# Kernel optimization log

Hardware: AMD Instinct MI355X
Metric: run time of the kernel (lower is better)

The kernel has to match this reference:

```python
import jax, jax.numpy as jnp
import numpy as np

B, T, N = 1024, 256, 64  # batch, seq_len, n_labels


def setup_inputs() -> dict:
    key = jax.random.key(0)
    k1, k2, k3, k4, k5 = jax.random.split(key, 5)
    emit = jax.random.normal(k1, (B, T, N), dtype=jnp.float32)
    lens = jax.random.randint(k2, (B,), T // 2, T + 1)
    mask = jnp.arange(T)[None, :] < lens[:, None]  # [B, T] bool, monotone
    trans = 0.1 * jax.random.normal(k3, (N, N), dtype=jnp.float32)
    strans = 0.1 * jax.random.normal(k4, (N,), dtype=jnp.float32)
    etrans = 0.1 * jax.random.normal(k5, (N,), dtype=jnp.float32)
    return {"emit": emit, "trans": trans, "strans": strans,
            "etrans": etrans, "mask": mask}


def reference(emit, trans, strans, etrans, mask):
    """CRF partition function (Tagger.get_logZ), summed over the batch."""
    lse = jax.scipy.special.logsumexp
    # row-normalize transitions in log space (as in the torch module)
    strans_n = strans - lse(strans)
    etrans_n = etrans - lse(etrans)
    trans_n = trans - lse(trans, axis=-1, keepdims=True)  # [N, N]

    e = jnp.transpose(emit, (1, 0, 2))  # [T, B, N]
    m = mask.T                          # [T, B]

    alpha0 = strans_n + e[0]            # [B, N]

    def step(alpha, xs):
        emit_t, mask_t = xs             # [B, N], [B]
        # scores[b, k] = logsumexp_j(alpha[b, j] + trans[j, k] + emit_t[b, k])
        scores = lse(alpha[:, :, None] + trans_n[None, :, :]
                     + emit_t[:, None, :], axis=1)
        alpha = jnp.where(mask_t[:, None], scores, alpha)
        return alpha, None

    alpha, _ = jax.lax.scan(step, alpha0, (e[1:], m[1:]))
    logZ = jnp.sum(lse(alpha + etrans_n, axis=1))
    return logZ
```

## Files before the change

### kernel.cpp

```cpp
#include <hip/hip_runtime.h>


#define CRF_B 1024
#define CRF_T 256
#define CRF_N 64

typedef __bf16 bf16x2 __attribute__((ext_vector_type(2)));

__device__ __forceinline__ float rl0(float x) {
    return __int_as_float(__builtin_amdgcn_readfirstlane(__float_as_int(x)));
}
__device__ __forceinline__ float rlanef(float x, int j) {
    return __int_as_float(__builtin_amdgcn_readlane(__float_as_int(x), j));
}

__device__ __forceinline__ float wave_lse(float v) {
    float m = v;
    #pragma unroll
    for (int off = 1; off < 64; off <<= 1) m = fmaxf(m, __shfl_xor(m, off));
    float s = __expf(v - m);
    #pragma unroll
    for (int off = 1; off < 64; off <<= 1) s += __shfl_xor(s, off);
    return m + __logf(s);
}

__device__ __forceinline__ unsigned bf16_rne(float f) {
    unsigned u = __float_as_uint(f);
    return (u + 0x7FFFu + ((u >> 16) & 1u)) >> 16;
}

__device__ __forceinline__ unsigned pack_pairs(float u) {
    unsigned pa = __float_as_uint(u) + 0x8000u;
    unsigned pb = (unsigned)__builtin_amdgcn_update_dpp(
        0, (int)pa, 0xB1 , 0xF, 0xF, false);
    return __builtin_amdgcn_perm(pb, pa, 0x07060302);
}

__device__ __forceinline__ float dot2bf(unsigned a, unsigned b, float c) {
#if __has_builtin(__builtin_amdgcn_fdot2_f32_bf16)
    return __builtin_amdgcn_fdot2_f32_bf16(__builtin_bit_cast(bf16x2, a),
                                           __builtin_bit_cast(bf16x2, b),
                                           c, false);
#else
    float d = c;
    asm("v_dot2_f32_bf16 %0, %1, %2, %0" : "+v"(d) : "v"(a), "v"(b));
    return d;
#endif
}

__launch_bounds__(64, 1)
__global__ void crf_fwd_kernel(const float* __restrict__ emit,
                               const float* __restrict__ trans,
                               const float* __restrict__ strans,
                               const float* __restrict__ etrans,
                               const unsigned char* __restrict__ mask_u8,
                               float* __restrict__ out)
{
    const int lane = threadIdx.x;
    const int b    = blockIdx.x;

    float rowlse_v;
    {
        const float* rowp = trans + lane * CRF_N;
        float m = -1e30f;
        #pragma unroll 8
        for (int k = 0; k < CRF_N; ++k) m = fmaxf(m, rowp[k]);
        float s = 0.f;
        #pragma unroll 8
        for (int k = 0; k < CRF_N; ++k) s += __expf(rowp[k] - m);
        rowlse_v = m + __logf(s);
    }

    float cmx = -1e30f;
    #pragma unroll
    for (int j = 0; j < CRF_N; ++j)
        cmx = fmaxf(cmx, trans[j * CRF_N + lane] - rlanef(rowlse_v, j));

    unsigned Epk[32];
    #pragma unroll
    for (int m = 0; m < 32; ++m) {
        float e0 = __expf(trans[(2 * m)     * CRF_N + lane] - rlanef(rowlse_v, 2 * m)     - cmx);
        float e1 = __expf(trans[(2 * m + 1) * CRF_N + lane] - rlanef(rowlse_v, 2 * m + 1) - cmx);
        Epk[m] = bf16_rne(e0) | (bf16_rne(e1) << 16);
    }

    const float sn = wave_lse(strans[lane]);

    int len;
    {
        int c8 = 0;
        #pragma unroll
        for (int q = 0; q < 4; ++q)
            c8 += (mask_u8[(size_t)b * CRF_T + q * 64 + lane] != 0) ? 1 : 0;
        for (int off = 1; off < 64; off <<= 1) c8 += __shfl_xor(c8, off);
        if (c8 >= 128) {
            len = c8;
        } else {
            const int* mi = (const int*)mask_u8;
            int ci = 0;
            #pragma unroll
            for (int q = 0; q < 4; ++q)
                ci += (mi[(size_t)b * CRF_T + q * 64 + lane] != 0) ? 1 : 0;
            for (int off = 1; off < 64; off <<= 1) ci += __shfl_xor(ci, off);
            len = ci;
        }
    }

    const float* eb = emit + (size_t)b * CRF_T * CRF_N;

    float alpha0 = (strans[lane] - sn) + eb[lane];
    float c0 = rl0(alpha0);
    float u  = __expf(alpha0 - c0);
    unsigned upi = pack_pairs(u);
    float R  = 1.0f;
    float Pm = 1.0f;
    int   Eacc = 0;

#define CRF_STEP(EE, EE0)                                                   \
    {                                                                       \
        float ree = R * (EE);               \
        float sc0 = R * (EE0);                                              \
        float a0 = 0.f, a1 = 0.f, a2 = 0.f, a3 = 0.f;                       \
        _Pragma("unroll")                                                   \
        for (int m2 = 0; m2 < 32; m2 += 4) {                                \
            unsigned w0 = (unsigned)__builtin_amdgcn_readlane((int)upi, 2 * m2 + 0); \
            unsigned w1 = (unsigned)__builtin_amdgcn_readlane((int)upi, 2 * m2 + 2); \
            unsigned w2 = (unsigned)__builtin_amdgcn_readlane((int)upi, 2 * m2 + 4); \
            unsigned w3 = (unsigned)__builtin_amdgcn_readlane((int)upi, 2 * m2 + 6); \
            a0 = dot2bf(w0, Epk[m2 + 0], a0);                               \
            a1 = dot2bf(w1, Epk[m2 + 1], a1);                               \
            a2 = dot2bf(w2, Epk[m2 + 2], a2);                               \
            a3 = dot2bf(w3, Epk[m2 + 3], a3);                               \
        }                                                                   \
        float s = (a0 + a1) + (a2 + a3);                                    \
        float s0 = rl0(s);                                                  \
        u = s * ree;                                                        \
        upi = pack_pairs(u);                                                \
        float u0 = s0 * sc0;              \
        R = __builtin_amdgcn_rcpf(u0);                                      \
        Pm *= u0;                                                           \
    }

    float eN[4], eeC[4], ee0C[4];
    #pragma unroll
    for (int d = 0; d < 4; ++d) eN[d] = eb[(size_t)(1 + d) * CRF_N + lane];
    #pragma unroll
    for (int d = 0; d < 4; ++d) eeC[d] = __expf(eN[d] + cmx);
    #pragma unroll
    for (int d = 0; d < 4; ++d) ee0C[d] = rl0(eeC[d]);

    int t0 = 1;
    while (t0 + 4 <= len) {
        #pragma unroll
        for (int d = 0; d < 4; ++d) {
            int ti = t0 + 4 + d;
            ti = (ti < len) ? ti : (len - 1);
            eN[d] = eb[(size_t)ti * CRF_N + lane];
        }
        CRF_STEP(eeC[0], ee0C[0]); CRF_STEP(eeC[1], ee0C[1]);
        CRF_STEP(eeC[2], ee0C[2]); CRF_STEP(eeC[3], ee0C[3]);
        {
            int ex;
            Pm = frexpf(Pm, &ex);
            Eacc += ex;
        }
        #pragma unroll
        for (int d = 0; d < 4; ++d) eeC[d] = __expf(eN[d] + cmx);
        #pragma unroll
        for (int d = 0; d < 4; ++d) ee0C[d] = rl0(eeC[d]);
        t0 += 4;
    }
    {
        const int nrem = len - t0;
        #pragma unroll
        for (int d = 0; d < 4; ++d) {
            if (d >= nrem) break;
            CRF_STEP(eeC[d], ee0C[d]);
        }
    }
#undef CRF_STEP

    const float en = wave_lse(etrans[lane]);
    float Lacc = c0 + 0.6931471805599453f * (float)Eacc + __logf(Pm);
    float v = Lacc + __logf(u * R) + (etrans[lane] - en);
    float m = v;
    #pragma unroll
    for (int off = 1; off < 64; off <<= 1) m = fmaxf(m, __shfl_xor(m, off));
    float sum = __expf(v - m);
    #pragma unroll
    for (int off = 1; off < 64; off <<= 1) sum += __shfl_xor(sum, off);

    if (lane == 0) {
        atomicAdd(out, m + __logf(sum));
    }
}

extern "C" void kernel_launch(void* const* d_in, const int* in_sizes, int n_in,
                              void* d_out, int out_size, void* d_ws, size_t ws_size,
                              hipStream_t stream) {
    const float* emit   = (const float*)d_in[0];
    const float* trans  = (const float*)d_in[1];
    const float* strans = (const float*)d_in[2];
    const float* etrans = (const float*)d_in[3];
    const unsigned char* mask = (const unsigned char*)d_in[4];
    float* out = (float*)d_out;

    hipMemsetAsync(out, 0, sizeof(float), stream);
    crf_fwd_kernel<<<dim3(CRF_B), dim3(64), 0, stream>>>(
        emit, trans, strans, etrans, mask, out);
}
```

Measured before the change: 142.7 us.

## Process two batch sequences per wave with interleaved recurrence chains

Each 64-lane block now handles two batch elements and interleaves their forward recurrences step by step, with per-sequence liveness predicates and a loop bound of the longer length. The goal is to hide the latency of the serial readlane/dot/pack chain by giving the scheduler two independent dependency chains. In exchange, half as many waves are launched, so fewer SIMDs may be busy. Steps are also wasted on the shorter sequence of each pair.

Result: slower. 190.7 us (+33.7%).

```diff
diff --git a/kernel.cpp b/kernel.cpp
--- a/kernel.cpp
+++ b/kernel.cpp
@@ -48,6 +48,25 @@
 #endif
 }
 
+__device__ __forceinline__ int seq_len(const unsigned char* __restrict__ mask_u8,
+                                       int b, int lane) {
+    int c8 = 0;
+    #pragma unroll
+    for (int q = 0; q < 4; ++q)
+        c8 += (mask_u8[(size_t)b * CRF_T + q * 64 + lane] != 0) ? 1 : 0;
+    #pragma unroll
+    for (int off = 1; off < 64; off <<= 1) c8 += __shfl_xor(c8, off);
+    if (c8 >= 128) return c8;
+    const int* mi = (const int*)mask_u8;
+    int ci = 0;
+    #pragma unroll
+    for (int q = 0; q < 4; ++q)
+        ci += (mi[(size_t)b * CRF_T + q * 64 + lane] != 0) ? 1 : 0;
+    #pragma unroll
+    for (int off = 1; off < 64; off <<= 1) ci += __shfl_xor(ci, off);
+    return ci;
+}
+
 __launch_bounds__(64, 1)
 __global__ void crf_fwd_kernel(const float* __restrict__ emit,
                                const float* __restrict__ trans,
@@ -57,7 +76,8 @@
                                float* __restrict__ out)
 {
     const int lane = threadIdx.x;
-    const int b    = blockIdx.x;
+    const int bA   = blockIdx.x * 2;
+    const int bB   = bA + 1;
 
     float rowlse_v;
     {
@@ -86,47 +106,35 @@
 
     const float sn = wave_lse(strans[lane]);
 
-    int len;
-    {
-        int c8 = 0;
-        #pragma unroll
-        for (int q = 0; q < 4; ++q)
-            c8 += (mask_u8[(size_t)b * CRF_T + q * 64 + lane] != 0) ? 1 : 0;
-        for (int off = 1; off < 64; off <<= 1) c8 += __shfl_xor(c8, off);
-        if (c8 >= 128) {
-            len = c8;
-        } else {
-            const int* mi = (const int*)mask_u8;
-            int ci = 0;
-            #pragma unroll
-            for (int q = 0; q < 4; ++q)
-                ci += (mi[(size_t)b * CRF_T + q * 64 + lane] != 0) ? 1 : 0;
-            for (int off = 1; off < 64; off <<= 1) ci += __shfl_xor(ci, off);
-            len = ci;
-        }
-    }
-
-    const float* eb = emit + (size_t)b * CRF_T * CRF_N;
-
-    float alpha0 = (strans[lane] - sn) + eb[lane];
-    float c0 = rl0(alpha0);
-    float u  = __expf(alpha0 - c0);
-    unsigned upi = pack_pairs(u);
-    float R  = 1.0f;
-    float Pm = 1.0f;
-    int   Eacc = 0;
-
-#define CRF_STEP(EE, EE0)                                                   \
+    const int lenA = seq_len(mask_u8, bA, lane);
+    const int lenB = seq_len(mask_u8, bB, lane);
+    const int lenMax = (lenA > lenB) ? lenA : lenB;
+
+    const float* ebA = emit + (size_t)bA * CRF_T * CRF_N;
+    const float* ebB = emit + (size_t)bB * CRF_T * CRF_N;
+
+    float alpha0A = (strans[lane] - sn) + ebA[lane];
+    float alpha0B = (strans[lane] - sn) + ebB[lane];
+    float c0A = rl0(alpha0A), c0B = rl0(alpha0B);
+    float uA = __expf(alpha0A - c0A);
+    float uB = __expf(alpha0B - c0B);
+    unsigned upiA = pack_pairs(uA);
+    unsigned upiB = pack_pairs(uB);
+    float RA = 1.0f, RB = 1.0f;
+    float PmA = 1.0f, PmB = 1.0f;
+    int   EaccA = 0, EaccB = 0;
+
+#define CRF_STEP(SFX, EE, EE0, LIVE)                                        \
     {                                                                       \
-        float ree = R * (EE);               \
-        float sc0 = R * (EE0);                                              \
+        float ree = R##SFX * (EE);          \
+        float sc0 = R##SFX * (EE0);                                         \
         float a0 = 0.f, a1 = 0.f, a2 = 0.f, a3 = 0.f;                       \
         _Pragma("unroll")                                                   \
         for (int m2 = 0; m2 < 32; m2 += 4) {                                \
-            unsigned w0 = (unsigned)__builtin_amdgcn_readlane((int)upi, 2 * m2 + 0); \
-            unsigned w1 = (unsigned)__builtin_amdgcn_readlane((int)upi, 2 * m2 + 2); \
-            unsigned w2 = (unsigned)__builtin_amdgcn_readlane((int)upi, 2 * m2 + 4); \
-            unsigned w3 = (unsigned)__builtin_amdgcn_readlane((int)upi, 2 * m2 + 6); \
+            unsigned w0 = (unsigned)__builtin_amdgcn_readlane((int)upi##SFX, 2 * m2 + 0); \
+            unsigned w1 = (unsigned)__builtin_amdgcn_readlane((int)upi##SFX, 2 * m2 + 2); \
+            unsigned w2 = (unsigned)__builtin_amdgcn_readlane((int)upi##SFX, 2 * m2 + 4); \
+            unsigned w3 = (unsigned)__builtin_amdgcn_readlane((int)upi##SFX, 2 * m2 + 6); \
             a0 = dot2bf(w0, Epk[m2 + 0], a0);                               \
             a1 = dot2bf(w1, Epk[m2 + 1], a1);                               \
             a2 = dot2bf(w2, Epk[m2 + 2], a2);                               \
@@ -134,64 +142,92 @@
         }                                                                   \
         float s = (a0 + a1) + (a2 + a3);                                    \
         float s0 = rl0(s);                                                  \
-        u = s * ree;                                                        \
-        upi = pack_pairs(u);                                                \
-        float u0 = s0 * sc0;              \
-        R = __builtin_amdgcn_rcpf(u0);                                      \
-        Pm *= u0;                                                           \
-    }
-
-    float eN[4], eeC[4], ee0C[4];
-    #pragma unroll
-    for (int d = 0; d < 4; ++d) eN[d] = eb[(size_t)(1 + d) * CRF_N + lane];
-    #pragma unroll
-    for (int d = 0; d < 4; ++d) eeC[d] = __expf(eN[d] + cmx);
-    #pragma unroll
-    for (int d = 0; d < 4; ++d) ee0C[d] = rl0(eeC[d]);
+        float u0 = s0 * sc0;                        \
+        const bool lv_ = (LIVE);                                            \
+        u##SFX  = lv_ ? (s * ree) : u##SFX;                                 \
+        R##SFX  = lv_ ? __builtin_amdgcn_rcpf(u0) : R##SFX;                 \
+        Pm##SFX *= lv_ ? u0 : 1.0f;                                         \
+        upi##SFX = pack_pairs(u##SFX);                                      \
+    }
+
+    float eNA[4], eeCA[4], ee0CA[4];
+    float eNB[4], eeCB[4], ee0CB[4];
+    #pragma unroll
+    for (int d = 0; d < 4; ++d) {
+        eNA[d] = ebA[(size_t)(1 + d) * CRF_N + lane];
+        eNB[d] = ebB[(size_t)(1 + d) * CRF_N + lane];
+    }
+    #pragma unroll
+    for (int d = 0; d < 4; ++d) { eeCA[d] = __expf(eNA[d] + cmx); eeCB[d] = __expf(eNB[d] + cmx); }
+    #pragma unroll
+    for (int d = 0; d < 4; ++d) { ee0CA[d] = rl0(eeCA[d]); ee0CB[d] = rl0(eeCB[d]); }
 
     int t0 = 1;
-    while (t0 + 4 <= len) {
+    while (t0 + 4 <= lenMax) {
         #pragma unroll
         for (int d = 0; d < 4; ++d) {
-            int ti = t0 + 4 + d;
-            ti = (ti < len) ? ti : (len - 1);
-            eN[d] = eb[(size_t)ti * CRF_N + lane];
+            int tiA = t0 + 4 + d; tiA = (tiA < lenA) ? tiA : (lenA - 1);
+            eNA[d] = ebA[(size_t)tiA * CRF_N + lane];
+            int tiB = t0 + 4 + d; tiB = (tiB < lenB) ? tiB : (lenB - 1);
+            eNB[d] = ebB[(size_t)tiB * CRF_N + lane];
         }
-        CRF_STEP(eeC[0], ee0C[0]); CRF_STEP(eeC[1], ee0C[1]);
-        CRF_STEP(eeC[2], ee0C[2]); CRF_STEP(eeC[3], ee0C[3]);
+        CRF_STEP(A, eeCA[0], ee0CA[0], t0 + 0 < lenA);
+        CRF_STEP(B, eeCB[0], ee0CB[0], t0 + 0 < lenB);
+        CRF_STEP(A, eeCA[1], ee0CA[1], t0 + 1 < lenA);
+        CRF_STEP(B, eeCB[1], ee0CB[1], t0 + 1 < lenB);
+        CRF_STEP(A, eeCA[2], ee0CA[2], t0 + 2 < lenA);
+        CRF_STEP(B, eeCB[2], ee0CB[2], t0 + 2 < lenB);
+        CRF_STEP(A, eeCA[3], ee0CA[3], t0 + 3 < lenA);
+        CRF_STEP(B, eeCB[3], ee0CB[3], t0 + 3 < lenB);
         {
             int ex;
-            Pm = frexpf(Pm, &ex);
-            Eacc += ex;
+            PmA = frexpf(PmA, &ex); EaccA += ex;
+            PmB = frexpf(PmB, &ex); EaccB += ex;
         }
         #pragma unroll
-        for (int d = 0; d < 4; ++d) eeC[d] = __expf(eN[d] + cmx);
-        #pragma unroll
-        for (int d = 0; d < 4; ++d) ee0C[d] = rl0(eeC[d]);
+        for (int d = 0; d < 4; ++d) { eeCA[d] = __expf(eNA[d] + cmx); eeCB[d] = __expf(eNB[d] + cmx); }
+        #pragma unroll
+        for (int d = 0; d < 4; ++d) { ee0CA[d] = rl0(eeCA[d]); ee0CB[d] = rl0(eeCB[d]); }
         t0 += 4;
     }
     {
-        const int nrem = len - t0;
+        const int nrem = lenMax - t0;
         #pragma unroll
         for (int d = 0; d < 4; ++d) {
             if (d >= nrem) break;
-            CRF_STEP(eeC[d], ee0C[d]);
+            CRF_STEP(A, eeCA[d], ee0CA[d], t0 + d < lenA);
+            CRF_STEP(B, eeCB[d], ee0CB[d], t0 + d < lenB);
         }
     }
 #undef CRF_STEP
 
     const float en = wave_lse(etrans[lane]);
-    float Lacc = c0 + 0.6931471805599453f * (float)Eacc + __logf(Pm);
-    float v = Lacc + __logf(u * R) + (etrans[lane] - en);
-    float m = v;
-    #pragma unroll
-    for (int off = 1; off < 64; off <<= 1) m = fmaxf(m, __shfl_xor(m, off));
-    float sum = __expf(v - m);
-    #pragma unroll
-    for (int off = 1; off < 64; off <<= 1) sum += __shfl_xor(sum, off);
+    float z = 0.f;
+    {
+        float Lacc = c0A + 0.6931471805599453f * (float)EaccA + __logf(PmA);
+        float v = Lacc + __logf(uA * RA) + (etrans[lane] - en);
+        float m = v;
+        #pragma unroll
+        for (int off = 1; off < 64; off <<= 1) m = fmaxf(m, __shfl_xor(m, off));
+        float sum = __expf(v - m);
+        #pragma unroll
+        for (int off = 1; off < 64; off <<= 1) sum += __shfl_xor(sum, off);
+        z += m + __logf(sum);
+    }
+    {
+        float Lacc = c0B + 0.6931471805599453f * (float)EaccB + __logf(PmB);
+        float v = Lacc + __logf(uB * RB) + (etrans[lane] - en);
+        float m = v;
+        #pragma unroll
+        for (int off = 1; off < 64; off <<= 1) m = fmaxf(m, __shfl_xor(m, off));
+        float sum = __expf(v - m);
+        #pragma unroll
+        for (int off = 1; off < 64; off <<= 1) sum += __shfl_xor(sum, off);
+        z += m + __logf(sum);
+    }
 
     if (lane == 0) {
-        atomicAdd(out, m + __logf(sum));
+        atomicAdd(out, z);
     }
 }
 
@@ -206,6 +242,6 @@
     float* out = (float*)d_out;
 
     hipMemsetAsync(out, 0, sizeof(float), stream);
-    crf_fwd_kernel<<<dim3(CRF_B), dim3(64), 0, stream>>>(
+    crf_fwd_kernel<<<dim3(CRF_B / 2), dim3(64), 0, stream>>>(
         emit, trans, strans, etrans, mask, out);
 }
```
